# Optimization experiments

Measured on AMD Instinct MI355X. Metric: run time of the kernel, lower is better.

The kernel has to match this reference:

```python
import jax, jax.numpy as jnp
import numpy as np

B, Q, P, H, W = 4, 64, 32, 512, 512
IDENTITY_ALPHA_EPSILON = 0.001


def setup_inputs() -> dict:
    key = jax.random.key(0)
    k1, k2, k3, k4, k5 = jax.random.split(key, 5)
    patch_alpha = jax.random.uniform(k1, (B, Q, P, P), dtype=jnp.float32)            # sigmoid-like in [0,1]
    centers = jax.random.uniform(k2, (B, Q, 2), dtype=jnp.float32) * 2.0 - 1.0       # tanh range
    depth = jax.random.uniform(k3, (B, Q, 1), dtype=jnp.float32) * 5.0               # sigmoid*5
    sizes = jax.random.uniform(k4, (B, Q, 2), dtype=jnp.float32) * 0.08 + 0.015      # sigmoid*0.08+0.015
    depth_scale = jax.random.uniform(k5, (B, Q, 1), dtype=jnp.float32)
    return {"patch_alpha": patch_alpha, "centers": centers, "depth": depth,
            "sizes": sizes, "depth_scale": depth_scale}


def _grid_sample_bilinear_zeros(img, ix, iy):
    # img: [N,h,w]; ix,iy: pixel coords [N,H,W]; bilinear, zero padding, align_corners=True
    h, w = img.shape[-2], img.shape[-1]
    x0f = jnp.floor(ix)
    y0f = jnp.floor(iy)
    wx = ix - x0f
    wy = iy - y0f
    x0 = x0f.astype(jnp.int32)
    y0 = y0f.astype(jnp.int32)
    n_idx = jnp.arange(img.shape[0])[:, None, None]

    def gather(yc, xc):
        valid = (xc >= 0) & (xc < w) & (yc >= 0) & (yc < h)
        v = img[n_idx, jnp.clip(yc, 0, h - 1), jnp.clip(xc, 0, w - 1)]
        return v * valid.astype(img.dtype)

    v00 = gather(y0, x0)
    v01 = gather(y0, x0 + 1)
    v10 = gather(y0 + 1, x0)
    v11 = gather(y0 + 1, x0 + 1)
    return (v00 * (1 - wx) * (1 - wy) + v01 * wx * (1 - wy)
            + v10 * (1 - wx) * wy + v11 * wx * wy)


def reference(patch_alpha, centers, depth, sizes, depth_scale):
    b, q, ph, pw = patch_alpha.shape
    ys = jnp.linspace(-1.0, 1.0, H)
    xs = jnp.linspace(-1.0, 1.0, W)
    gy, gx = jnp.meshgrid(ys, xs, indexing='ij')                    # [H,W]
    cx = centers[..., 0][:, :, None, None]
    cy = centers[..., 1][:, :, None, None]
    sx = sizes[..., 0][:, :, None, None]
    sy = sizes[..., 1][:, :, None, None]
    lx = jnp.clip((gx - cx) / sx, -1.1, 1.1)                        # [B,Q,H,W]
    ly = jnp.clip((gy - cy) / sy, -1.1, 1.1)
    # normalized -> pixel coords (align_corners=True)
    ix = (lx + 1.0) * 0.5 * (pw - 1)
    iy = (ly + 1.0) * 0.5 * (ph - 1)
    sampled = _grid_sample_bilinear_zeros(
        patch_alpha.reshape(b * q, ph, pw),
        ix.reshape(b * q, H, W), iy.reshape(b * q, H, W)).reshape(b, q, H, W)

    # depth sort, far -> near (descending)
    order = jnp.argsort(-depth[..., 0], axis=1)                      # [B,Q]
    sorted_alpha = jnp.take_along_axis(sampled, order[:, :, None, None], axis=1)
    sorted_depth = jnp.take_along_axis(depth[..., 0], order, axis=1) # [B,Q]
    ident_vals = (order + 1).astype(sampled.dtype)                   # [B,Q]

    # transmittance recurrence as exclusive cumprod of (1-alpha)
    t = jnp.cumprod(1.0 - sorted_alpha, axis=1)                      # [B,Q,H,W]
    t_excl = jnp.concatenate([jnp.ones_like(t[:, :1]), t[:, :-1]], axis=1)
    contrib = sorted_alpha * t_excl                                  # alpha * T before this query

    rendered_depth = jnp.sum(contrib * sorted_depth[:, :, None, None], axis=1)  # [B,H,W]

    hit = contrib > IDENTITY_ALPHA_EPSILON
    first = jnp.argmax(hit, axis=1)                                  # first query (in sorted order) to assign
    any_hit = jnp.any(hit, axis=1)
    identity = ident_vals[jnp.arange(b)[:, None, None], first]       # [B,H,W]
    rendered_identity = jnp.where(any_hit, identity, jnp.zeros((), sampled.dtype))

    occ = jnp.clip(1.0 - t[:, -1], 0.0, 1.0)                         # [B,H,W]
    vis = (occ > 0.05).astype(sampled.dtype)
    rendered_identity = rendered_identity * vis
    rendered_depth = rendered_depth * vis
    rendered_depth = rendered_depth[:, None] * jnp.mean(depth_scale, axis=1, keepdims=True)[..., None]
    return rendered_identity, rendered_depth, occ[:, None]
```

## Files before the change

kernel.cpp:

```cpp
#include <hip/hip_runtime.h>

#define QN 64
#define PATCH 32
#define HH 512
#define WW 512
#define NPIX (4 * 512 * 512)

__global__ __launch_bounds__(256) void render_kernel(
    const float* __restrict__ patch,
    const float* __restrict__ centers,
    const float* __restrict__ depth,
    const float* __restrict__ sizes,
    const float* __restrict__ dscale,
    float* __restrict__ out)
{
#pragma clang fp contract(off)
    const int tid = threadIdx.x;
    const int b   = blockIdx.z;
    const int x   = (blockIdx.x << 4) + (tid & 15);
    const int y   = (blockIdx.y << 4) + (tid >> 4);

    __shared__ float sp[QN][8];
    __shared__ float sdep[QN];
    __shared__ int   slist[QN];
    __shared__ int   scount;
    __shared__ float smean;

    if (tid < QN) sdep[tid] = depth[(b << 6) + tid];
    __syncthreads();

    if (tid < QN) {
        const float d = sdep[tid];
        int rank = 0;
#pragma unroll
        for (int j = 0; j < QN; ++j) {
            const float dj = sdep[j];
            rank += ((dj > d) || ((dj == d) && (j < tid))) ? 1 : 0;
        }
        const int gi = (b << 6) + tid;
        sp[rank][0] = centers[gi * 2 + 0];
        sp[rank][1] = centers[gi * 2 + 1];
        sp[rank][2] = sizes[gi * 2 + 0];
        sp[rank][3] = sizes[gi * 2 + 1];
        sp[rank][4] = d;
        sp[rank][5] = (float)(tid + 1);
        sp[rank][6] = __int_as_float(tid);

        float v = dscale[gi];
        for (int off = 32; off; off >>= 1) v += __shfl_down(v, off);
        if (tid == 0) smean = v * (1.0f / 64.0f);
    }
    __syncthreads();

    const float STEP = 2.0f / 511.0f;

    if (tid < QN) {
        const float gx_lo = -1.0f + (float)(blockIdx.x << 4) * STEP;
        const float gx_hi = -1.0f + (float)((blockIdx.x << 4) + 15) * STEP;
        const float gy_lo = -1.0f + (float)(blockIdx.y << 4) * STEP;
        const float gy_hi = -1.0f + (float)((blockIdx.y << 4) + 15) * STEP;
        const float C = 1.0660f;
        const float cx = sp[tid][0], cy = sp[tid][1];
        const float sxv = sp[tid][2], syv = sp[tid][3];
        const bool keep = (cx + C * sxv >= gx_lo) && (cx - C * sxv <= gx_hi) &&
                          (cy + C * syv >= gy_lo) && (cy - C * syv <= gy_hi);
        const unsigned long long m = __ballot(keep);
        if (keep) slist[__popcll(m & ((1ull << tid) - 1ull))] = tid;
        if (tid == 0) scount = (int)__popcll(m);
    }
    __syncthreads();

    const float gx = -1.0f + (float)x * STEP;
    const float gy = -1.0f + (float)y * STEP;

    float t = 1.0f;
    float dep = 0.0f;
    float identv = 0.0f;
    bool  anyhit = false;
    const int cnt = scount;

    for (int i = 0; i < cnt; ++i) {
        const int q = slist[i];
        const float cx = sp[q][0], cy = sp[q][1];
        const float sxv = sp[q][2], syv = sp[q][3];
        const float dq = sp[q][4], iv = sp[q][5];
        const int pq = __float_as_int(sp[q][6]);

        float lx = (gx - cx) / sxv;
        lx = fminf(fmaxf(lx, -1.1f), 1.1f);
        float ly = (gy - cy) / syv;
        ly = fminf(fmaxf(ly, -1.1f), 1.1f);
        const float ix = (lx + 1.0f) * 0.5f * 31.0f;
        const float iy = (ly + 1.0f) * 0.5f * 31.0f;
        const float x0f = floorf(ix), y0f = floorf(iy);
        const float wx = ix - x0f, wy = iy - y0f;
        const int x0 = (int)x0f, y0 = (int)y0f;

        const float* pp = patch + (((size_t)(b << 6) + (size_t)pq) << 10);
        const bool xok0 = (x0 >= 0) && (x0 < PATCH);
        const bool xok1 = (x0 + 1 >= 0) && (x0 + 1 < PATCH);
        const bool yok0 = (y0 >= 0) && (y0 < PATCH);
        const bool yok1 = (y0 + 1 >= 0) && (y0 + 1 < PATCH);
        const float v00 = (xok0 && yok0) ? pp[(y0 << 5) + x0] : 0.0f;
        const float v01 = (xok1 && yok0) ? pp[(y0 << 5) + x0 + 1] : 0.0f;
        const float v10 = (xok0 && yok1) ? pp[((y0 + 1) << 5) + x0] : 0.0f;
        const float v11 = (xok1 && yok1) ? pp[((y0 + 1) << 5) + x0 + 1] : 0.0f;

        const float a = v00 * (1.0f - wx) * (1.0f - wy)
                      + v01 * wx * (1.0f - wy)
                      + v10 * (1.0f - wx) * wy
                      + v11 * wx * wy;

        const float contrib = a * t;
        if (!anyhit && (contrib > 0.001f)) { anyhit = true; identv = iv; }
        dep += contrib * dq;
        t *= (1.0f - a);
    }

    float occ = 1.0f - t;
    occ = fminf(fmaxf(occ, 0.0f), 1.0f);
    const float vis = (occ > 0.05f) ? 1.0f : 0.0f;
    float ido = anyhit ? identv : 0.0f;
    ido *= vis;
    const float dpo = (dep * vis) * smean;

    const size_t pix = (((size_t)b * HH) + (size_t)y) * WW + (size_t)x;
    out[pix] = ido;
    out[(size_t)NPIX + pix] = dpo;
    out[2 * (size_t)NPIX + pix] = occ;
}

extern "C" void kernel_launch(void* const* d_in, const int* in_sizes, int n_in,
                              void* d_out, int out_size, void* d_ws, size_t ws_size,
                              hipStream_t stream) {
    const float* patch   = (const float*)d_in[0];
    const float* centers = (const float*)d_in[1];
    const float* depth   = (const float*)d_in[2];
    const float* sizes   = (const float*)d_in[3];
    const float* dscale  = (const float*)d_in[4];
    float* out = (float*)d_out;

    dim3 grid(WW / 16, HH / 16, 4);
    render_kernel<<<grid, 256, 0, stream>>>(patch, centers, depth, sizes, dscale, out);
}
```

Measured before the change: 16.04 us.

## Render 4 pixels per thread on 32x32 tiles with float4 stores and shuffle-based sort

Each thread now handles four adjacent pixels in a row, and each block covers a 32x32 tile instead of 16x16. Per-query y-coordinate work and setup are shared across the four pixels, and the outputs are written with float4 stores. The depth ranking now uses wavefront shuffles instead of a shared-memory array, which removes one barrier. The trade-off is coarser tile culling: larger tiles keep more queries per block, and the grid drops to 1024 blocks, which may lower occupancy or increase the number of patch samples.

```diff
diff --git a/kernel.cpp b/kernel.cpp
--- a/kernel.cpp
+++ b/kernel.cpp
@@ -17,31 +17,36 @@
 #pragma clang fp contract(off)
     const int tid = threadIdx.x;
     const int b   = blockIdx.z;
-    const int x   = (blockIdx.x << 4) + (tid & 15);
-    const int y   = (blockIdx.y << 4) + (tid >> 4);
+    const int tx0 = blockIdx.x << 5;
+    const int ty0 = blockIdx.y << 5;
+    const int xp  = tx0 + ((tid & 7) << 2);
+    const int y   = ty0 + (tid >> 3);
 
     __shared__ float sp[QN][8];
-    __shared__ float sdep[QN];
     __shared__ int   slist[QN];
     __shared__ int   scount;
     __shared__ float smean;
 
-    if (tid < QN) sdep[tid] = depth[(b << 6) + tid];
-    __syncthreads();
+    const float STEP = 2.0f / 511.0f;
 
     if (tid < QN) {
-        const float d = sdep[tid];
+        const int gi = (b << 6) + tid;
+        const float d   = depth[gi];
+        const float cx0 = centers[gi * 2 + 0];
+        const float cy0 = centers[gi * 2 + 1];
+        const float sx0 = sizes[gi * 2 + 0];
+        const float sy0 = sizes[gi * 2 + 1];
+
         int rank = 0;
 #pragma unroll
         for (int j = 0; j < QN; ++j) {
-            const float dj = sdep[j];
+            const float dj = __shfl(d, j);
             rank += ((dj > d) || ((dj == d) && (j < tid))) ? 1 : 0;
         }
-        const int gi = (b << 6) + tid;
-        sp[rank][0] = centers[gi * 2 + 0];
-        sp[rank][1] = centers[gi * 2 + 1];
-        sp[rank][2] = sizes[gi * 2 + 0];
-        sp[rank][3] = sizes[gi * 2 + 1];
+        sp[rank][0] = cx0;
+        sp[rank][1] = cy0;
+        sp[rank][2] = sx0;
+        sp[rank][3] = sy0;
         sp[rank][4] = d;
         sp[rank][5] = (float)(tid + 1);
         sp[rank][6] = __int_as_float(tid);
@@ -49,16 +54,11 @@
         float v = dscale[gi];
         for (int off = 32; off; off >>= 1) v += __shfl_down(v, off);
         if (tid == 0) smean = v * (1.0f / 64.0f);
-    }
-    __syncthreads();
 
-    const float STEP = 2.0f / 511.0f;
-
-    if (tid < QN) {
-        const float gx_lo = -1.0f + (float)(blockIdx.x << 4) * STEP;
-        const float gx_hi = -1.0f + (float)((blockIdx.x << 4) + 15) * STEP;
-        const float gy_lo = -1.0f + (float)(blockIdx.y << 4) * STEP;
-        const float gy_hi = -1.0f + (float)((blockIdx.y << 4) + 15) * STEP;
+        const float gx_lo = -1.0f + (float)tx0 * STEP;
+        const float gx_hi = -1.0f + (float)(tx0 + 31) * STEP;
+        const float gy_lo = -1.0f + (float)ty0 * STEP;
+        const float gy_hi = -1.0f + (float)(ty0 + 31) * STEP;
         const float C = 1.0660f;
         const float cx = sp[tid][0], cy = sp[tid][1];
         const float sxv = sp[tid][2], syv = sp[tid][3];
@@ -70,64 +70,78 @@
     }
     __syncthreads();
 
-    const float gx = -1.0f + (float)x * STEP;
+    const int cnt = scount;
     const float gy = -1.0f + (float)y * STEP;
+    float gx[4];
+#pragma unroll
+    for (int k = 0; k < 4; ++k) gx[k] = -1.0f + (float)(xp + k) * STEP;
 
-    float t = 1.0f;
-    float dep = 0.0f;
-    float identv = 0.0f;
-    bool  anyhit = false;
-    const int cnt = scount;
+    float tr[4]  = {1.0f, 1.0f, 1.0f, 1.0f};
+    float dp[4]  = {0.0f, 0.0f, 0.0f, 0.0f};
+    float idv[4] = {0.0f, 0.0f, 0.0f, 0.0f};
+    int hitm = 0;
 
     for (int i = 0; i < cnt; ++i) {
         const int q = slist[i];
-        const float cx = sp[q][0], cy = sp[q][1];
+        const float cx  = sp[q][0], cy  = sp[q][1];
         const float sxv = sp[q][2], syv = sp[q][3];
-        const float dq = sp[q][4], iv = sp[q][5];
-        const int pq = __float_as_int(sp[q][6]);
+        const float dq  = sp[q][4], iv  = sp[q][5];
+        const int   pq  = __float_as_int(sp[q][6]);
+        const float* pp = patch + (((size_t)((b << 6) + pq)) << 10);
 
-        float lx = (gx - cx) / sxv;
-        lx = fminf(fmaxf(lx, -1.1f), 1.1f);
         float ly = (gy - cy) / syv;
         ly = fminf(fmaxf(ly, -1.1f), 1.1f);
-        const float ix = (lx + 1.0f) * 0.5f * 31.0f;
-        const float iy = (ly + 1.0f) * 0.5f * 31.0f;
-        const float x0f = floorf(ix), y0f = floorf(iy);
-        const float wx = ix - x0f, wy = iy - y0f;
-        const int x0 = (int)x0f, y0 = (int)y0f;
+        const float iy  = (ly + 1.0f) * 0.5f * 31.0f;
+        const float y0f = floorf(iy);
+        const float wy  = iy - y0f;
+        const int   yi  = (int)y0f;
+        const bool yok0 = (yi >= 0) && (yi < PATCH);
+        const bool yok1 = (yi + 1 >= 0) && (yi + 1 < PATCH);
+        const int row0 = yi << 5, row1 = (yi + 1) << 5;
 
-        const float* pp = patch + (((size_t)(b << 6) + (size_t)pq) << 10);
-        const bool xok0 = (x0 >= 0) && (x0 < PATCH);
-        const bool xok1 = (x0 + 1 >= 0) && (x0 + 1 < PATCH);
-        const bool yok0 = (y0 >= 0) && (y0 < PATCH);
-        const bool yok1 = (y0 + 1 >= 0) && (y0 + 1 < PATCH);
-        const float v00 = (xok0 && yok0) ? pp[(y0 << 5) + x0] : 0.0f;
-        const float v01 = (xok1 && yok0) ? pp[(y0 << 5) + x0 + 1] : 0.0f;
-        const float v10 = (xok0 && yok1) ? pp[((y0 + 1) << 5) + x0] : 0.0f;
-        const float v11 = (xok1 && yok1) ? pp[((y0 + 1) << 5) + x0 + 1] : 0.0f;
+#pragma unroll
+        for (int k = 0; k < 4; ++k) {
+            float lx = (gx[k] - cx) / sxv;
+            lx = fminf(fmaxf(lx, -1.1f), 1.1f);
+            const float ixf = (lx + 1.0f) * 0.5f * 31.0f;
+            const float x0f = floorf(ixf);
+            const float wx  = ixf - x0f;
+            const int   xi  = (int)x0f;
+            const bool xok0 = (xi >= 0) && (xi < PATCH);
+            const bool xok1 = (xi + 1 >= 0) && (xi + 1 < PATCH);
+            const float v00 = (xok0 && yok0) ? pp[row0 + xi] : 0.0f;
+            const float v01 = (xok1 && yok0) ? pp[row0 + xi + 1] : 0.0f;
+            const float v10 = (xok0 && yok1) ? pp[row1 + xi] : 0.0f;
+            const float v11 = (xok1 && yok1) ? pp[row1 + xi + 1] : 0.0f;
 
-        const float a = v00 * (1.0f - wx) * (1.0f - wy)
-                      + v01 * wx * (1.0f - wy)
-                      + v10 * (1.0f - wx) * wy
-                      + v11 * wx * wy;
+            const float a = v00 * (1.0f - wx) * (1.0f - wy)
+                          + v01 * wx * (1.0f - wy)
+                          + v10 * (1.0f - wx) * wy
+                          + v11 * wx * wy;
 
-        const float contrib = a * t;
-        if (!anyhit && (contrib > 0.001f)) { anyhit = true; identv = iv; }
-        dep += contrib * dq;
-        t *= (1.0f - a);
+            const float contrib = a * tr[k];
+            if (!(hitm & (1 << k)) && (contrib > 0.001f)) { hitm |= (1 << k); idv[k] = iv; }
+            dp[k] += contrib * dq;
+            tr[k] *= (1.0f - a);
+        }
     }
 
-    float occ = 1.0f - t;
-    occ = fminf(fmaxf(occ, 0.0f), 1.0f);
-    const float vis = (occ > 0.05f) ? 1.0f : 0.0f;
-    float ido = anyhit ? identv : 0.0f;
-    ido *= vis;
-    const float dpo = (dep * vis) * smean;
+    const float sm = smean;
+    float4 o_id, o_dp, o_oc;
+#pragma unroll
+    for (int k = 0; k < 4; ++k) {
+        float occ = 1.0f - tr[k];
+        occ = fminf(fmaxf(occ, 0.0f), 1.0f);
+        const float vis = (occ > 0.05f) ? 1.0f : 0.0f;
+        ((float*)&o_id)[k] = idv[k] * vis;
+        ((float*)&o_dp)[k] = (dp[k] * vis) * sm;
+        ((float*)&o_oc)[k] = occ;
+    }
 
-    const size_t pix = (((size_t)b * HH) + (size_t)y) * WW + (size_t)x;
-    out[pix] = ido;
-    out[(size_t)NPIX + pix] = dpo;
-    out[2 * (size_t)NPIX + pix] = occ;
+    const size_t pix = ((size_t)b * HH + (size_t)y) * WW + (size_t)xp;
+    *(float4*)(out + pix)                    = o_id;
+    *(float4*)(out + (size_t)NPIX + pix)     = o_dp;
+    *(float4*)(out + 2 * (size_t)NPIX + pix) = o_oc;
 }
 
 extern "C" void kernel_launch(void* const* d_in, const int* in_sizes, int n_in,
@@ -140,6 +154,6 @@
     const float* dscale  = (const float*)d_in[4];
     float* out = (float*)d_out;
 
-    dim3 grid(WW / 16, HH / 16, 4);
+    dim3 grid(WW / 32, HH / 32, 4);
     render_kernel<<<grid, 256, 0, stream>>>(patch, centers, depth, sizes, dscale, out);
 }
```

New measurement: 15.48 us. 1.04x faster.
